# Performance work log

Measured on AMD Instinct MI355X. Metric: run time of the kernel, lower is better.

The kernel has to match this reference:

```python
import jax, jax.numpy as jnp
import numpy as np

N_HEADS = 4
HEAD_DIM = 128
FMAP_H, FMAP_W = 32, 32
IN_DIM = 512
BATCH = 16


def setup_inputs() -> dict:
    key = jax.random.key(0)
    k1, k2, k3, k4 = jax.random.split(key, 4)
    scale = HEAD_DIM ** (-0.5)
    x = jax.random.normal(k1, (BATCH, IN_DIM, FMAP_H, FMAP_W), dtype=jnp.float32)
    # 1x1 conv weight producing q,k,v stacked along output channels
    conv_w = jax.random.normal(k2, (3 * N_HEADS * HEAD_DIM, IN_DIM), dtype=jnp.float32) * (IN_DIM ** -0.5)
    pos_h = jax.random.normal(k3, (FMAP_H, HEAD_DIM), dtype=jnp.float32) * scale
    pos_w = jax.random.normal(k4, (FMAP_W, HEAD_DIM), dtype=jnp.float32) * scale
    return {"x": x, "conv_w": conv_w, "pos_h": pos_h, "pos_w": pos_w}


def reference(x, conv_w, pos_h, pos_w):
    B, C, H, W = x.shape
    hw = H * W
    scale = HEAD_DIM ** (-0.5)
    # 1x1 conv == pointwise linear over channels
    qkv = jnp.einsum('bchw,oc->bohw', x, conv_w)               # [B, 3*nh*hd, H, W]
    qkv = qkv.reshape(B, 3, N_HEADS, HEAD_DIM, hw)             # chunk + per-head split
    q = jnp.swapaxes(qkv[:, 0], -1, -2) * scale                # [B, nh, hw, hd]
    k = jnp.swapaxes(qkv[:, 1], -1, -2)
    v = jnp.swapaxes(qkv[:, 2], -1, -2)
    # absolute positional embedding: h[i,:]+w[j,:] flattened over positions
    emb = (pos_h[:, None, :] + pos_w[None, :, :]).reshape(hw, HEAD_DIM)
    sim = jnp.einsum('bhid,bhjd->bhij', q, k) + jnp.einsum('bhid,jd->bhij', q, emb)
    attn = jax.nn.softmax(sim, axis=-1)
    out = jnp.einsum('bhij,bhjd->bhid', attn, v)               # [B, nh, hw, hd]
    out = jnp.swapaxes(out, -1, -2)                            # [B, nh, hd, hw]
    return out.reshape(B, N_HEADS * HEAD_DIM, hw // N_HEADS, N_HEADS)
```

## Files before the change

kernel.cpp:

```cpp
#include <hip/hip_runtime.h>

#define NB 16
#define NH 4
#define HD 128
#define HW 1024
#define CIN 512

typedef short s16x8 __attribute__((ext_vector_type(8)));
typedef short s16x4 __attribute__((ext_vector_type(4)));
typedef float f32x4 __attribute__((ext_vector_type(4)));

static __device__ __forceinline__ short f2bf(float f) {
    union { float f; unsigned u; } v; v.f = f;
    unsigned r = v.u + 0x7fffu + ((v.u >> 16) & 1u);
    return (short)(r >> 16);
}

__global__ __launch_bounds__(256) void prep_xw(
    const float* __restrict__ x, const float* __restrict__ w,
    short* __restrict__ xT, short* __restrict__ Wb)
{
    int blk = blockIdx.x;
    if (blk < NB * 16 * 32) {
        int b = blk >> 9, rem = blk & 511;
        int ct = rem >> 5, pt = rem & 31;
        __shared__ float tile[32][33];
        int tc = threadIdx.x >> 5;
        int tp = threadIdx.x & 31;
        const float* xb = x + ((size_t)b * CIN + ct * 32) * HW + pt * 32;
        #pragma unroll
        for (int i = 0; i < 4; i++)
            tile[tc + i * 8][tp] = xb[(size_t)(tc + i * 8) * HW + tp];
        __syncthreads();
        int p = threadIdx.x >> 3, cq = threadIdx.x & 7;
        short* xo = xT + ((size_t)b * HW + pt * 32 + p) * CIN + ct * 32 + cq * 4;
        s16x4 o4 = { f2bf(tile[cq * 4 + 0][p]), f2bf(tile[cq * 4 + 1][p]),
                     f2bf(tile[cq * 4 + 2][p]), f2bf(tile[cq * 4 + 3][p]) };
        *reinterpret_cast<s16x4*>(xo) = o4;
    } else {
        int wb = blk - NB * 16 * 32;
        size_t base = (size_t)wb * 1024 + threadIdx.x * 4;
        const float4 v = *reinterpret_cast<const float4*>(w + base);
        s16x4 o4 = { f2bf(v.x), f2bf(v.y), f2bf(v.z), f2bf(v.w) };
        *reinterpret_cast<s16x4*>(Wb + base) = o4;
    }
}

__global__ __launch_bounds__(256, 3) void qkv_proj(
    const short* __restrict__ xT, const short* __restrict__ Wb,
    const float* __restrict__ pos_h, const float* __restrict__ pos_w,
    short* __restrict__ Q, short* __restrict__ Kp, short* __restrict__ Vt)
{
    __shared__ __align__(16) char smem[34816];
    short* As = (short*)smem;
    short* Bs = As + 128 * 64;
    short* vb = (short*)smem;

    const int pt = blockIdx.x, ot = blockIdx.y, b = blockIdx.z;
    const int tid = threadIdx.x;
    const int wave = tid >> 6, lane = tid & 63;
    const int l16 = lane & 15, quad = lane >> 4;
    const int wm = (wave & 1) * 64, wn = (wave >> 1) * 64;
    const int o0 = ot * 128, p0 = pt * 128;

    const short* xb = xT + (size_t)b * HW * CIN;

    const int r0 = tid >> 3, c0 = tid & 7;
    const int sphys = c0 ^ (r0 & 7);
    const short* wp = Wb + (size_t)(o0 + r0) * CIN + c0 * 8;
    const short* xp = xb + (size_t)(p0 + r0) * CIN + c0 * 8;
    short* adst = As + r0 * 64 + sphys * 8;
    short* bdst = Bs + r0 * 64 + sphys * 8;

    f32x4 acc[4][4];
    #pragma unroll
    for (int i = 0; i < 4; i++)
        #pragma unroll
        for (int j = 0; j < 4; j++)
            acc[i][j] = f32x4{0.f, 0.f, 0.f, 0.f};

    s16x8 wreg[4], xreg[4];
    #pragma unroll
    for (int p = 0; p < 4; p++) {
        wreg[p] = *(const s16x8*)(wp + (size_t)(p * 32) * CIN);
        xreg[p] = *(const s16x8*)(xp + (size_t)(p * 32) * CIN);
    }

    #pragma unroll 1
    for (int kc = 0; kc < CIN; kc += 64) {
        #pragma unroll
        for (int p = 0; p < 4; p++) {
            *(s16x8*)(adst + p * 32 * 64) = wreg[p];
            *(s16x8*)(bdst + p * 32 * 64) = xreg[p];
        }
        __syncthreads();
        int kcn = (kc + 64) & (CIN - 1);
        #pragma unroll
        for (int p = 0; p < 4; p++) {
            wreg[p] = *(const s16x8*)(wp + kcn + (size_t)(p * 32) * CIN);
            xreg[p] = *(const s16x8*)(xp + kcn + (size_t)(p * 32) * CIN);
        }
        #pragma unroll
        for (int kk = 0; kk < 2; kk++) {
            s16x8 aF[4], bF[4];
            #pragma unroll
            for (int mi = 0; mi < 4; mi++)
                aF[mi] = *(const s16x8*)(As + (wm + mi * 16 + l16) * 64
                                         + (((kk * 4 + quad) ^ (l16 & 7)) * 8));
            #pragma unroll
            for (int ni = 0; ni < 4; ni++)
                bF[ni] = *(const s16x8*)(Bs + (wn + ni * 16 + l16) * 64
                                         + (((kk * 4 + quad) ^ (l16 & 7)) * 8));
            #pragma unroll
            for (int mi = 0; mi < 4; mi++)
                #pragma unroll
                for (int ni = 0; ni < 4; ni++)
                    acc[mi][ni] = __builtin_amdgcn_mfma_f32_16x16x32_bf16(
                        aF[mi], bF[ni], acc[mi][ni], 0, 0, 0);
        }
        __syncthreads();
    }

    const int s = ot >> 2, h = ot & 3;
    const size_t bh = (size_t)(b * NH + h);

    if (s == 0) {
        const float qs = 0.08838834764831845f * 1.4426950408889634f;
        short* Qb = Q + bh * (size_t)(HW * HD);
        #pragma unroll
        for (int mi = 0; mi < 4; mi++) {
            int d0 = wm + mi * 16 + quad * 4;
            #pragma unroll
            for (int ni = 0; ni < 4; ni++) {
                int p = p0 + wn + ni * 16 + l16;
                f32x4 a = acc[mi][ni];
                s16x4 o4 = { f2bf(a.x * qs), f2bf(a.y * qs),
                             f2bf(a.z * qs), f2bf(a.w * qs) };
                *reinterpret_cast<s16x4*>(Qb + (size_t)p * HD + d0) = o4;
            }
        }
    } else if (s == 1) {
        short* Kb = Kp + bh * (size_t)(HW * HD);
        #pragma unroll
        for (int mi = 0; mi < 4; mi++) {
            int d0 = wm + mi * 16 + quad * 4;
            #pragma unroll
            for (int ni = 0; ni < 4; ni++) {
                int p = p0 + wn + ni * 16 + l16;
                const float4 eh = *reinterpret_cast<const float4*>(pos_h + (p >> 5) * HD + d0);
                const float4 ew = *reinterpret_cast<const float4*>(pos_w + (p & 31) * HD + d0);
                f32x4 a = acc[mi][ni];
                s16x4 o4 = { f2bf(a.x + eh.x + ew.x), f2bf(a.y + eh.y + ew.y),
                             f2bf(a.z + eh.z + ew.z), f2bf(a.w + eh.w + ew.w) };
                *reinterpret_cast<s16x4*>(Kb + (size_t)p * HD + d0) = o4;
            }
        }
    } else {
        __syncthreads();
        #pragma unroll
        for (int mi = 0; mi < 4; mi++) {
            int d0 = wm + mi * 16 + quad * 4;
            #pragma unroll
            for (int ni = 0; ni < 4; ni++) {
                int p = wn + ni * 16 + l16;
                f32x4 a = acc[mi][ni];
                vb[(d0 + 0) * 136 + p] = f2bf(a.x);
                vb[(d0 + 1) * 136 + p] = f2bf(a.y);
                vb[(d0 + 2) * 136 + p] = f2bf(a.z);
                vb[(d0 + 3) * 136 + p] = f2bf(a.w);
            }
        }
        __syncthreads();
        short* Vb = Vt + bh * (size_t)(HD * HW);
        int d = tid >> 1, half = tid & 1;
        #pragma unroll
        for (int j = 0; j < 8; j++) {
            s16x8 v8 = *(const s16x8*)(vb + d * 136 + half * 64 + j * 8);
            *reinterpret_cast<s16x8*>(Vb + (size_t)d * HW + p0 + half * 64 + j * 8) = v8;
        }
    }
}

__global__ __launch_bounds__(256, 2) void attn_fused(
    const short* __restrict__ Q, const short* __restrict__ Kp,
    const short* __restrict__ Vt, float* __restrict__ out)
{
    __shared__ short Ks[64 * 128];
    __shared__ short Vs[128 * 64];
    __shared__ short Ps[4 * 32 * 64];

    const int flat = blockIdx.x;
    const int qt = flat >> 6;
    const int bh = flat & 63;
    const int tid = threadIdx.x;
    const int wave = tid >> 6, lane = tid & 63;
    const int l16 = lane & 15, quad = lane >> 4;

    const short* Qb = Q + (size_t)bh * (HW * HD);
    const short* Kb = Kp + (size_t)bh * (HW * HD);
    const short* Vb = Vt + (size_t)bh * (HD * HW);
    short* myP = Ps + wave * (32 * 64);

    const int q0 = qt * 128 + wave * 32;

    s16x8 bQ[2][4];
    #pragma unroll
    for (int nt = 0; nt < 2; nt++)
        #pragma unroll
        for (int kk = 0; kk < 4; kk++)
            bQ[nt][kk] = *(const s16x8*)(Qb + (size_t)(q0 + nt * 16 + l16) * HD
                                         + kk * 32 + quad * 8);

    s16x8 ones;
    #pragma unroll
    for (int j = 0; j < 8; j++) ones[j] = (short)0x3F80;

    f32x4 Oacc[2][8];
    #pragma unroll
    for (int mt = 0; mt < 2; mt++)
        #pragma unroll
        for (int dt = 0; dt < 8; dt++)
            Oacc[mt][dt] = f32x4{0.f, 0.f, 0.f, 0.f};
    f32x4 lacc[2] = { f32x4{0.f, 0.f, 0.f, 0.f}, f32x4{0.f, 0.f, 0.f, 0.f} };

    const int kKey = tid >> 4, kC = tid & 15;
    const int kPhys = kC ^ kKey;
    const short* kgp = Kb + (size_t)kKey * HD + kC * 8;
    short* kdst = Ks + kKey * 128 + kPhys * 8;
    const int vD = tid >> 3, vC = tid & 7;
    const int vPhys = vC ^ (vD & 7);
    const short* vgp = Vb + (size_t)vD * HW + vC * 8;
    short* vdst = Vs + vD * 64 + vPhys * 8;

    s16x8 kreg[4], vreg[4];
    #pragma unroll
    for (int i = 0; i < 4; i++) {
        kreg[i] = *(const s16x8*)(kgp + (size_t)(i * 16) * HD);
        vreg[i] = *(const s16x8*)(vgp + (size_t)(i * 32) * HW);
    }

    #pragma unroll 1
    for (int kt = 0; kt < 16; kt++) {
        #pragma unroll
        for (int i = 0; i < 4; i++) {
            *(s16x8*)(kdst + i * 16 * 128) = kreg[i];
            *(s16x8*)(vdst + i * 32 * 64) = vreg[i];
        }
        __syncthreads();

        int ktn = (kt + 1) & 15;
        #pragma unroll
        for (int i = 0; i < 4; i++) {
            kreg[i] = *(const s16x8*)(kgp + (size_t)(ktn * 64 + i * 16) * HD);
            vreg[i] = *(const s16x8*)(vgp + ktn * 64 + (size_t)(i * 32) * HW);
        }

        f32x4 c[4][2];
        #pragma unroll
        for (int mtp = 0; mtp < 4; mtp++) {
            s16x8 aK[4];
            #pragma unroll
            for (int kk = 0; kk < 4; kk++)
                aK[kk] = *(const s16x8*)(Ks + (mtp * 16 + l16) * 128
                                         + (((kk * 4 + quad) ^ l16) * 8));
            c[mtp][0] = f32x4{0.f, 0.f, 0.f, 0.f};
            c[mtp][1] = f32x4{0.f, 0.f, 0.f, 0.f};
            #pragma unroll
            for (int kk = 0; kk < 4; kk++) {
                c[mtp][0] = __builtin_amdgcn_mfma_f32_16x16x32_bf16(
                    aK[kk], bQ[0][kk], c[mtp][0], 0, 0, 0);
                c[mtp][1] = __builtin_amdgcn_mfma_f32_16x16x32_bf16(
                    aK[kk], bQ[1][kk], c[mtp][1], 0, 0, 0);
            }
        }

        #pragma unroll
        for (int mtp = 0; mtp < 4; mtp++)
            #pragma unroll
            for (int nt = 0; nt < 2; nt++) {
                f32x4 pv = c[mtp][nt];
                s16x4 pp = { f2bf(__builtin_amdgcn_exp2f(pv[0])),
                             f2bf(__builtin_amdgcn_exp2f(pv[1])),
                             f2bf(__builtin_amdgcn_exp2f(pv[2])),
                             f2bf(__builtin_amdgcn_exp2f(pv[3])) };
                int q = nt * 16 + l16;
                int chunk = 2 * mtp + (quad >> 1);
                int phys = chunk ^ (l16 & 7);
                *(s16x4*)(myP + q * 64 + phys * 8 + (quad & 1) * 4) = pp;
            }

        s16x8 aP[2][2];
        #pragma unroll
        for (int mt = 0; mt < 2; mt++)
            #pragma unroll
            for (int kp = 0; kp < 2; kp++) {
                int phys = (kp * 4 + quad) ^ (l16 & 7);
                aP[mt][kp] = *(const s16x8*)(myP + (mt * 16 + l16) * 64 + phys * 8);
            }

        #pragma unroll
        for (int mt = 0; mt < 2; mt++)
            #pragma unroll
            for (int kp = 0; kp < 2; kp++)
                lacc[mt] = __builtin_amdgcn_mfma_f32_16x16x32_bf16(
                    aP[mt][kp], ones, lacc[mt], 0, 0, 0);

        #pragma unroll
        for (int dt = 0; dt < 8; dt++) {
            s16x8 bV0 = *(const s16x8*)(Vs + (dt * 16 + l16) * 64
                                        + ((quad ^ (l16 & 7)) * 8));
            s16x8 bV1 = *(const s16x8*)(Vs + (dt * 16 + l16) * 64
                                        + (((4 + quad) ^ (l16 & 7)) * 8));
            #pragma unroll
            for (int mt = 0; mt < 2; mt++) {
                Oacc[mt][dt] = __builtin_amdgcn_mfma_f32_16x16x32_bf16(
                    aP[mt][0], bV0, Oacc[mt][dt], 0, 0, 0);
                Oacc[mt][dt] = __builtin_amdgcn_mfma_f32_16x16x32_bf16(
                    aP[mt][1], bV1, Oacc[mt][dt], 0, 0, 0);
            }
        }
        __syncthreads();
    }

    float* ob = out + (size_t)bh * (HD * HW);
    #pragma unroll
    for (int mt = 0; mt < 2; mt++) {
        float inv[4];
        #pragma unroll
        for (int r = 0; r < 4; r++) inv[r] = __builtin_amdgcn_rcpf(lacc[mt][r]);
        int prow = q0 + mt * 16 + quad * 4;
        #pragma unroll
        for (int dt = 0; dt < 8; dt++) {
            int d = dt * 16 + l16;
            f32x4 o = Oacc[mt][dt];
            float4 o4 = { o[0] * inv[0], o[1] * inv[1],
                          o[2] * inv[2], o[3] * inv[3] };
            *reinterpret_cast<float4*>(ob + (size_t)d * HW + prow) = o4;
        }
    }
}

extern "C" void kernel_launch(void* const* d_in, const int* in_sizes, int n_in,
                              void* d_out, int out_size, void* d_ws, size_t ws_size,
                              hipStream_t stream) {
    const float* x  = (const float*)d_in[0];
    const float* w  = (const float*)d_in[1];
    const float* ph = (const float*)d_in[2];
    const float* pw = (const float*)d_in[3];

    const size_t BHPD = (size_t)NB * NH * HW * HD;
    short* Q    = (short*)d_ws;
    short* Kp   = Q + BHPD;
    short* Vt   = Kp + BHPD;
    short* xT   = Vt + BHPD;
    short* Wb   = xT + (size_t)NB * HW * CIN;
    float* outp = (float*)d_out;

    prep_xw<<<dim3(NB * 16 * 32 + 768), 256, 0, stream>>>(x, w, xT, Wb);
    qkv_proj<<<dim3(8, 12, NB), 256, 0, stream>>>(xT, Wb, ph, pw, Q, Kp, Vt);
    attn_fused<<<dim3(512), 256, 0, stream>>>(Q, Kp, Vt, outp);
}
```

Before: 172.0 us.

## Use direct global-to-LDS loads with double buffering and pre-swizzled global layouts

Replaces the register-staged global-to-shared copies in the projection and attention kernels with async global_load_lds into double-buffered shared memory. So that these raw 16-byte copies land in the existing XOR-swizzled LDS layout, the producer kernels now write xT, Wb, K and Vt to global memory already swizzled. The goal is to overlap loading of the next tile with MFMA work and to free the staging registers. In exchange, shared memory use doubles, qkv_proj occupancy drops from 3 to 2 blocks per CU, and correctness depends on every producer and consumer agreeing on the swizzle.

```diff
diff --git a/kernel.cpp b/kernel.cpp
--- a/kernel.cpp
+++ b/kernel.cpp
@@ -14,6 +14,12 @@
     union { float f; unsigned u; } v; v.f = f;
     unsigned r = v.u + 0x7fffu + ((v.u >> 16) & 1u);
     return (short)(r >> 16);
+}
+
+static __device__ __forceinline__ void gld16(const short* g, short* l) {
+    __builtin_amdgcn_global_load_lds(
+        (const __attribute__((address_space(1))) void*)g,
+        (__attribute__((address_space(3))) void*)l, 16, 0, 0);
 }
 
 __global__ __launch_bounds__(256) void prep_xw(
@@ -33,7 +39,9 @@
             tile[tc + i * 8][tp] = xb[(size_t)(tc + i * 8) * HW + tp];
         __syncthreads();
         int p = threadIdx.x >> 3, cq = threadIdx.x & 7;
-        short* xo = xT + ((size_t)b * HW + pt * 32 + p) * CIN + ct * 32 + cq * 4;
+        int cc = ct * 4 + (cq >> 1);
+        int phys = (cc & ~7) | ((cc & 7) ^ (p & 7));
+        short* xo = xT + ((size_t)b * HW + pt * 32 + p) * CIN + phys * 8 + (cq & 1) * 4;
         s16x4 o4 = { f2bf(tile[cq * 4 + 0][p]), f2bf(tile[cq * 4 + 1][p]),
                      f2bf(tile[cq * 4 + 2][p]), f2bf(tile[cq * 4 + 3][p]) };
         *reinterpret_cast<s16x4*>(xo) = o4;
@@ -41,20 +49,22 @@
         int wb = blk - NB * 16 * 32;
         size_t base = (size_t)wb * 1024 + threadIdx.x * 4;
         const float4 v = *reinterpret_cast<const float4*>(w + base);
+        int o = (int)(base >> 9);
+        int col = (int)(base & 511);
+        int cc = col >> 3;
+        int phys = (cc & ~7) | ((cc & 7) ^ (o & 7));
         s16x4 o4 = { f2bf(v.x), f2bf(v.y), f2bf(v.z), f2bf(v.w) };
-        *reinterpret_cast<s16x4*>(Wb + base) = o4;
-    }
-}
-
-__global__ __launch_bounds__(256, 3) void qkv_proj(
+        *reinterpret_cast<s16x4*>(Wb + (size_t)o * 512 + phys * 8 + (col & 7)) = o4;
+    }
+}
+
+__global__ __launch_bounds__(256, 2) void qkv_proj(
     const short* __restrict__ xT, const short* __restrict__ Wb,
     const float* __restrict__ pos_h, const float* __restrict__ pos_w,
     short* __restrict__ Q, short* __restrict__ Kp, short* __restrict__ Vt)
 {
-    __shared__ __align__(16) char smem[34816];
-    short* As = (short*)smem;
-    short* Bs = As + 128 * 64;
-    short* vb = (short*)smem;
+    __shared__ __align__(16) short smem[32768];
+    short* vb = smem;
 
     const int pt = blockIdx.x, ot = blockIdx.y, b = blockIdx.z;
     const int tid = threadIdx.x;
@@ -64,13 +74,8 @@
     const int o0 = ot * 128, p0 = pt * 128;
 
     const short* xb = xT + (size_t)b * HW * CIN;
-
-    const int r0 = tid >> 3, c0 = tid & 7;
-    const int sphys = c0 ^ (r0 & 7);
-    const short* wp = Wb + (size_t)(o0 + r0) * CIN + c0 * 8;
-    const short* xp = xb + (size_t)(p0 + r0) * CIN + c0 * 8;
-    short* adst = As + r0 * 64 + sphys * 8;
-    short* bdst = Bs + r0 * 64 + sphys * 8;
+    const short* ag = Wb + (size_t)(o0 + (lane >> 3)) * CIN + (lane & 7) * 8;
+    const short* bg = xb + (size_t)(p0 + (lane >> 3)) * CIN + (lane & 7) * 8;
 
     f32x4 acc[4][4];
     #pragma unroll
@@ -79,27 +84,26 @@
         for (int j = 0; j < 4; j++)
             acc[i][j] = f32x4{0.f, 0.f, 0.f, 0.f};
 
-    s16x8 wreg[4], xreg[4];
-    #pragma unroll
-    for (int p = 0; p < 4; p++) {
-        wreg[p] = *(const s16x8*)(wp + (size_t)(p * 32) * CIN);
-        xreg[p] = *(const s16x8*)(xp + (size_t)(p * 32) * CIN);
-    }
+    auto stage = [&](int kc, int buf) {
+        short* Ad = smem + buf * 8192;
+        short* Bd = smem + 16384 + buf * 8192;
+        #pragma unroll
+        for (int j = 0; j < 4; j++) {
+            int rbase = j * 32 + wave * 8;
+            gld16(ag + (size_t)rbase * CIN + kc, Ad + rbase * 64);
+            gld16(bg + (size_t)rbase * CIN + kc, Bd + rbase * 64);
+        }
+    };
+
+    stage(0, 0);
+    __syncthreads();
 
     #pragma unroll 1
-    for (int kc = 0; kc < CIN; kc += 64) {
-        #pragma unroll
-        for (int p = 0; p < 4; p++) {
-            *(s16x8*)(adst + p * 32 * 64) = wreg[p];
-            *(s16x8*)(bdst + p * 32 * 64) = xreg[p];
-        }
-        __syncthreads();
-        int kcn = (kc + 64) & (CIN - 1);
-        #pragma unroll
-        for (int p = 0; p < 4; p++) {
-            wreg[p] = *(const s16x8*)(wp + kcn + (size_t)(p * 32) * CIN);
-            xreg[p] = *(const s16x8*)(xp + kcn + (size_t)(p * 32) * CIN);
-        }
+    for (int it = 0; it < 8; it++) {
+        int cb = it & 1;
+        if (it < 7) stage((it + 1) * 64, cb ^ 1);
+        const short* As = smem + cb * 8192;
+        const short* Bs = smem + 16384 + cb * 8192;
         #pragma unroll
         for (int kk = 0; kk < 2; kk++) {
             s16x8 aF[4], bF[4];
@@ -144,6 +148,7 @@
         #pragma unroll
         for (int mi = 0; mi < 4; mi++) {
             int d0 = wm + mi * 16 + quad * 4;
+            int lc = d0 >> 3;
             #pragma unroll
             for (int ni = 0; ni < 4; ni++) {
                 int p = p0 + wn + ni * 16 + l16;
@@ -152,7 +157,8 @@
                 f32x4 a = acc[mi][ni];
                 s16x4 o4 = { f2bf(a.x + eh.x + ew.x), f2bf(a.y + eh.y + ew.y),
                              f2bf(a.z + eh.z + ew.z), f2bf(a.w + eh.w + ew.w) };
-                *reinterpret_cast<s16x4*>(Kb + (size_t)p * HD + d0) = o4;
+                int phys = lc ^ l16;
+                *reinterpret_cast<s16x4*>(Kb + (size_t)p * HD + phys * 8 + (d0 & 7)) = o4;
             }
         }
     } else {
@@ -176,7 +182,8 @@
         #pragma unroll
         for (int j = 0; j < 8; j++) {
             s16x8 v8 = *(const s16x8*)(vb + d * 136 + half * 64 + j * 8);
-            *reinterpret_cast<s16x8*>(Vb + (size_t)d * HW + p0 + half * 64 + j * 8) = v8;
+            int pj = j ^ (d & 7);
+            *reinterpret_cast<s16x8*>(Vb + (size_t)d * HW + p0 + half * 64 + pj * 8) = v8;
         }
     }
 }
@@ -185,8 +192,8 @@
     const short* __restrict__ Q, const short* __restrict__ Kp,
     const short* __restrict__ Vt, float* __restrict__ out)
 {
-    __shared__ short Ks[64 * 128];
-    __shared__ short Vs[128 * 64];
+    __shared__ short Ks[2][64 * 128];
+    __shared__ short Vs[2][128 * 64];
     __shared__ short Ps[4 * 32 * 64];
 
     const int flat = blockIdx.x;
@@ -223,37 +230,31 @@
             Oacc[mt][dt] = f32x4{0.f, 0.f, 0.f, 0.f};
     f32x4 lacc[2] = { f32x4{0.f, 0.f, 0.f, 0.f}, f32x4{0.f, 0.f, 0.f, 0.f} };
 
-    const int kKey = tid >> 4, kC = tid & 15;
-    const int kPhys = kC ^ kKey;
-    const short* kgp = Kb + (size_t)kKey * HD + kC * 8;
-    short* kdst = Ks + kKey * 128 + kPhys * 8;
-    const int vD = tid >> 3, vC = tid & 7;
-    const int vPhys = vC ^ (vD & 7);
-    const short* vgp = Vb + (size_t)vD * HW + vC * 8;
-    short* vdst = Vs + vD * 64 + vPhys * 8;
-
-    s16x8 kreg[4], vreg[4];
-    #pragma unroll
-    for (int i = 0; i < 4; i++) {
-        kreg[i] = *(const s16x8*)(kgp + (size_t)(i * 16) * HD);
-        vreg[i] = *(const s16x8*)(vgp + (size_t)(i * 32) * HW);
-    }
+    const short* kg = Kb + (size_t)(lane >> 4) * HD + (lane & 15) * 8;
+    const short* vg = Vb + (size_t)(lane >> 3) * HW + (lane & 7) * 8;
+
+    auto stage = [&](int kt, int buf) {
+        #pragma unroll
+        for (int j = 0; j < 4; j++) {
+            int rbase = j * 16 + wave * 4;
+            gld16(kg + (size_t)(kt * 64 + rbase) * HD, &Ks[buf][rbase * 128]);
+        }
+        #pragma unroll
+        for (int j = 0; j < 4; j++) {
+            int dbase = j * 32 + wave * 8;
+            gld16(vg + (size_t)dbase * HW + kt * 64, &Vs[buf][dbase * 64]);
+        }
+    };
+
+    stage(0, 0);
+    __syncthreads();
 
     #pragma unroll 1
     for (int kt = 0; kt < 16; kt++) {
-        #pragma unroll
-        for (int i = 0; i < 4; i++) {
-            *(s16x8*)(kdst + i * 16 * 128) = kreg[i];
-            *(s16x8*)(vdst + i * 32 * 64) = vreg[i];
-        }
-        __syncthreads();
-
-        int ktn = (kt + 1) & 15;
-        #pragma unroll
-        for (int i = 0; i < 4; i++) {
-            kreg[i] = *(const s16x8*)(kgp + (size_t)(ktn * 64 + i * 16) * HD);
-            vreg[i] = *(const s16x8*)(vgp + ktn * 64 + (size_t)(i * 32) * HW);
-        }
+        int cb = kt & 1;
+        if (kt < 15) stage(kt + 1, cb ^ 1);
+        const short* KsC = &Ks[cb][0];
+        const short* VsC = &Vs[cb][0];
 
         f32x4 c[4][2];
         #pragma unroll
@@ -261,7 +262,7 @@
             s16x8 aK[4];
             #pragma unroll
             for (int kk = 0; kk < 4; kk++)
-                aK[kk] = *(const s16x8*)(Ks + (mtp * 16 + l16) * 128
+                aK[kk] = *(const s16x8*)(KsC + (mtp * 16 + l16) * 128
                                          + (((kk * 4 + quad) ^ l16) * 8));
             c[mtp][0] = f32x4{0.f, 0.f, 0.f, 0.f};
             c[mtp][1] = f32x4{0.f, 0.f, 0.f, 0.f};
@@ -307,9 +308,9 @@
 
         #pragma unroll
         for (int dt = 0; dt < 8; dt++) {
-            s16x8 bV0 = *(const s16x8*)(Vs + (dt * 16 + l16) * 64
+            s16x8 bV0 = *(const s16x8*)(VsC + (dt * 16 + l16) * 64
                                         + ((quad ^ (l16 & 7)) * 8));
-            s16x8 bV1 = *(const s16x8*)(Vs + (dt * 16 + l16) * 64
+            s16x8 bV1 = *(const s16x8*)(VsC + (dt * 16 + l16) * 64
                                         + (((4 + quad) ^ (l16 & 7)) * 8));
             #pragma unroll
             for (int mt = 0; mt < 2; mt++) {
```

New measurement: 172.9 us. Within noise of the previous version (+0.5%).
